# Kernel optimization log

Hardware: AMD Instinct MI355X
Metric: run time of the kernel (lower is better)

The kernel has to match this reference:

```python
import jax, jax.numpy as jnp
import numpy as np

NUM_HEAD = 8
EPS = 1e-12  # matches torch F.normalize default eps


def setup_inputs() -> dict:
    key = jax.random.key(0)
    k1, k2, k3 = jax.random.split(key, 3)
    B, N, C = 8, 8192, 384
    x = jax.random.normal(k1, (B, N, C), dtype=jnp.float32)
    # torch Linear weights: (out_features, in_features)
    w_qkv = jax.random.normal(k2, (3 * C, C), dtype=jnp.float32) * (C ** -0.5)
    w_proj = jax.random.normal(k3, (C, C), dtype=jnp.float32) * (C ** -0.5)
    b_proj = jnp.zeros((C,), dtype=jnp.float32)
    return {"x": x, "w_qkv": w_qkv, "w_proj": w_proj, "b_proj": b_proj}


def _l2norm(t):
    # F.normalize(t, dim=-1): t / max(||t||_2, eps)
    n = jnp.sqrt(jnp.sum(t * t, axis=-1, keepdims=True))
    return t / jnp.maximum(n, EPS)


def reference(x, w_qkv, w_proj, b_proj):
    B, N, C = x.shape
    H = NUM_HEAD
    Dh = C // H
    qkv = x @ w_qkv.T  # (B, N, 3C), qkv_bias=False
    qkv = qkv.reshape(B, N, 3, H, Dh).transpose(2, 0, 3, 1, 4)  # (3, B, H, N, Dh)
    q, k, v = qkv[0], qkv[1], qkv[2]
    # transpose(-2, -1) -> (B, H, Dh, N); normalize along N (cross-covariance attn)
    q = _l2norm(jnp.swapaxes(q, -2, -1))
    k = _l2norm(jnp.swapaxes(k, -2, -1))
    v = jnp.swapaxes(v, -2, -1)  # (B, H, Dh, N)
    attn = jnp.einsum('bhdn,bhen->bhde', q, k)  # (B, H, Dh, Dh)
    attn = jax.nn.softmax(attn, axis=-1)
    out = jnp.einsum('bhde,bhen->bhdn', attn, v)  # (B, H, Dh, N)
    out = out.transpose(0, 3, 1, 2).reshape(B, N, C)  # (B, N, C)
    out = out @ w_proj.T + b_proj
    return out
```

## Files before the change

### kernel.cpp

```cpp
#include <hip/hip_runtime.h>
#include <hip/hip_bf16.h>
#include <stdint.h>


typedef __bf16 bf16_t;
typedef __attribute__((ext_vector_type(8))) __bf16 bf16x8;
typedef __attribute__((ext_vector_type(4))) __bf16 bf16x4;
typedef __attribute__((ext_vector_type(4))) float f32x4;

#define NTOK 8192
#define CDIM 384
#define WH   25165824
#define DHN  393216

#define XCHUNKS 3145728
#define TCHUNKS 3201024

__device__ __forceinline__ f32x4 mfma16(bf16x8 a, bf16x8 b, f32x4 c) {
  return __builtin_amdgcn_mfma_f32_16x16x32_bf16(a, b, c, 0, 0, 0);
}

__device__ __forceinline__ void gload16(bf16_t* lds, const bf16_t* g) {
  __builtin_amdgcn_global_load_lds(
      (const __attribute__((address_space(1))) void*)g,
      (__attribute__((address_space(3))) void*)lds, 16, 0, 0);
}

template <bool BF16>
__device__ __forceinline__ bf16x8 load8(const void* p, int idx) {
  if constexpr (BF16) {
    return *(const bf16x8*)((const bf16_t*)p + idx);
  } else {
    const float* f = (const float*)p + idx;
    f32x4 a = *(const f32x4*)f;
    f32x4 b = *(const f32x4*)(f + 4);
    bf16x8 r;
    r[0] = (bf16_t)a[0]; r[1] = (bf16_t)a[1]; r[2] = (bf16_t)a[2]; r[3] = (bf16_t)a[3];
    r[4] = (bf16_t)b[0]; r[5] = (bf16_t)b[1]; r[6] = (bf16_t)b[2]; r[7] = (bf16_t)b[3];
    return r;
  }
}

__global__ void k_probe(const uint32_t* __restrict__ X, int* __restrict__ flag) {
  __shared__ int cnt;
  if (threadIdx.x == 0) cnt = 0;
  __syncthreads();
  const uint32_t w = X[threadIdx.x];
  const int e = (int)((w >> 7) & 0xFF);
  const int sane = (e >= 110 && e <= 131) ? 1 : 0;
  atomicAdd(&cnt, sane);
  __syncthreads();
  if (threadIdx.x == 0) *flag = (cnt >= 128) ? 1 : 0;
}

__global__ void k_zero(float* __restrict__ p, int n) {
  int i = blockIdx.x * 256 + threadIdx.x;
  if (i < n) p[i] = 0.f;
}

__global__ void k_cvt(const void* __restrict__ X, const void* __restrict__ Wqkv,
                      bf16_t* __restrict__ Xb, bf16_t* __restrict__ Wb,
                      const int* __restrict__ flagp) {
  const int isb = *flagp;
  const int G = gridDim.x * 256;
  for (int c = blockIdx.x * 256 + threadIdx.x; c < TCHUNKS; c += G) {
    const bool isX = c < XCHUNKS;
    const int lc = isX ? c : c - XCHUNKS;
    const void* src = isX ? X : Wqkv;
    bf16_t* dst = (isX ? Xb : Wb) + (size_t)lc * 8;
    if (isb) {
      *(bf16x8*)dst = *((const bf16x8*)src + lc);
    } else {
      const f32x4 a = *((const f32x4*)src + lc * 2);
      const f32x4 b = *((const f32x4*)src + lc * 2 + 1);
      bf16x8 r;
      r[0] = (bf16_t)a[0]; r[1] = (bf16_t)a[1]; r[2] = (bf16_t)a[2]; r[3] = (bf16_t)a[3];
      r[4] = (bf16_t)b[0]; r[5] = (bf16_t)b[1]; r[6] = (bf16_t)b[2]; r[7] = (bf16_t)b[3];
      *(bf16x8*)dst = r;
    }
  }
}

__device__ __forceinline__ void qkv_body_pipe(const bf16_t* __restrict__ XB,
                                              const bf16_t* __restrict__ WB,
                                              bf16_t* __restrict__ qkv,
                                              bf16_t* As, bf16_t* Bs) {
  const int tid = threadIdx.x;
  const int lane = tid & 63;
  const int wr = tid >> 7, wc = (tid >> 6) & 1;
  const int q4 = lane >> 4, l16 = lane & 15;
  const int rowB0 = blockIdx.x * 128;
  const int r0 = tid >> 2, kk = (tid & 3) << 3;
  const int bb = rowB0 >> 13;
  const int nB = rowB0 & 8191;

  auto STAGE = [&](int jts, int ks, int nxt) {
    const int rowA0 = jts * 128;
    const int k0 = ks * 32;
    bf16_t* Ad = As + nxt * 4096;
    bf16_t* Bd = Bs + nxt * 4096;
    gload16(Ad + tid * 8,         WB + (rowA0 + r0) * CDIM + k0 + kk);
    gload16(Ad + (tid + 256) * 8, WB + (rowA0 + r0 + 64) * CDIM + k0 + kk);
    gload16(Bd + tid * 8,         XB + (rowB0 + r0) * CDIM + k0 + kk);
    gload16(Bd + (tid + 256) * 8, XB + (rowB0 + r0 + 64) * CDIM + k0 + kk);
  };

  STAGE(0, 0, 0);
  __syncthreads();
  int cur = 0;

  for (int jt = 0; jt < 9; jt++) {
    const int which = jt / 3;
    const int jtt = jt - which * 3;
    f32x4 acc[4][4];
#pragma unroll
    for (int i = 0; i < 4; i++)
#pragma unroll
      for (int j = 0; j < 4; j++) acc[i][j] = (f32x4){0.f, 0.f, 0.f, 0.f};

    for (int k = 0; k < 12; k++) {
      if (!(jt == 8 && k == 11)) {
        int kn = k + 1, jn = jt;
        if (kn == 12) { kn = 0; jn = jt + 1; }
        STAGE(jn, kn, cur ^ 1);
      }
      const bf16_t* Ac = As + cur * 4096;
      const bf16_t* Bc = Bs + cur * 4096;
      bf16x8 af[4], bfr[4];
#pragma unroll
      for (int i = 0; i < 4; i++) {
        af[i]  = *(const bf16x8*)&Ac[(wr * 64 + i * 16 + l16) * 32 + q4 * 8];
        bfr[i] = *(const bf16x8*)&Bc[(wc * 64 + i * 16 + l16) * 32 + q4 * 8];
      }
      if (which < 2) {
#pragma unroll
        for (int i = 0; i < 4; i++)
#pragma unroll
          for (int j = 0; j < 4; j++) acc[i][j] = mfma16(bfr[j], af[i], acc[i][j]);
      } else {
#pragma unroll
        for (int i = 0; i < 4; i++)
#pragma unroll
          for (int j = 0; j < 4; j++) acc[i][j] = mfma16(af[i], bfr[j], acc[i][j]);
      }
      __syncthreads();
      cur ^= 1;
    }

    if (which < 2) {
#pragma unroll
      for (int i = 0; i < 4; i++) {
        const int rin = jtt * 128 + wr * 64 + i * 16 + l16;
        const int h = rin / 48, dh = rin - h * 48;
        bf16_t* rowp = qkv + which * WH + (bb * 8 + h) * DHN + dh * NTOK
                       + nB + wc * 64 + q4 * 4;
#pragma unroll
        for (int j = 0; j < 4; j++) {
          bf16x4 o = {(bf16_t)acc[i][j][0], (bf16_t)acc[i][j][1],
                      (bf16_t)acc[i][j][2], (bf16_t)acc[i][j][3]};
          *(bf16x4*)(rowp + j * 16) = o;
        }
      }
    } else {
#pragma unroll
      for (int i = 0; i < 4; i++) {
        const int rin0 = jtt * 128 + wr * 64 + i * 16 + q4 * 4;
#pragma unroll
        for (int j = 0; j < 4; j++) {
          const int mg = rowB0 + wc * 64 + j * 16 + l16;
          bf16x4 o = {(bf16_t)acc[i][j][0], (bf16_t)acc[i][j][1],
                      (bf16_t)acc[i][j][2], (bf16_t)acc[i][j][3]};
          *(bf16x4*)(qkv + 2 * WH + mg * CDIM + rin0) = o;
        }
      }
    }
  }
}

__global__ __launch_bounds__(256, 2) void k_gemm_qkv(
    const bf16_t* __restrict__ Xb, const bf16_t* __restrict__ Wb,
    bf16_t* __restrict__ qkv) {
  __shared__ __align__(16) bf16_t As[2 * 4096];
  __shared__ __align__(16) bf16_t Bs[2 * 4096];
  qkv_body_pipe(Xb, Wb, qkv, As, Bs);
}

template <bool BF16>
__device__ __forceinline__ void qkv_body_legacy(const void* __restrict__ X,
                                                const void* __restrict__ Wqkv,
                                                bf16_t* __restrict__ qkv,
                                                bf16_t* As, bf16_t* Bs) {
  const int tid = threadIdx.x;
  const int lane = tid & 63;
  const int wr = tid >> 7, wc = (tid >> 6) & 1;
  const int q4 = lane >> 4, l16 = lane & 15;
  const int rowB0 = blockIdx.x * 128;
  const int r0 = tid >> 2, kk = (tid & 3) << 3;
  const int bb = rowB0 >> 13;
  const int nB = rowB0 & 8191;

  for (int jt = 0; jt < 9; jt++) {
    const int rowA0 = jt * 128;
    const int which = jt / 3;
    const int jtt = jt - which * 3;
    f32x4 acc[4][4];
#pragma unroll
    for (int i = 0; i < 4; i++)
#pragma unroll
      for (int j = 0; j < 4; j++) acc[i][j] = (f32x4){0.f, 0.f, 0.f, 0.f};

    for (int k0 = 0; k0 < CDIM; k0 += 32) {
      bf16x8 a0 = load8<BF16>(Wqkv, (rowA0 + r0) * CDIM + k0 + kk);
      bf16x8 a1 = load8<BF16>(Wqkv, (rowA0 + r0 + 64) * CDIM + k0 + kk);
      bf16x8 b0 = load8<BF16>(X, (rowB0 + r0) * CDIM + k0 + kk);
      bf16x8 b1 = load8<BF16>(X, (rowB0 + r0 + 64) * CDIM + k0 + kk);
      __syncthreads();
      *(bf16x8*)&As[tid * 8] = a0;
      *(bf16x8*)&As[(tid + 256) * 8] = a1;
      *(bf16x8*)&Bs[tid * 8] = b0;
      *(bf16x8*)&Bs[(tid + 256) * 8] = b1;
      __syncthreads();
      bf16x8 af[4], bfr[4];
#pragma unroll
      for (int i = 0; i < 4; i++) {
        af[i]  = *(const bf16x8*)&As[(wr * 64 + i * 16 + l16) * 32 + q4 * 8];
        bfr[i] = *(const bf16x8*)&Bs[(wc * 64 + i * 16 + l16) * 32 + q4 * 8];
      }
      if (which < 2) {
#pragma unroll
        for (int i = 0; i < 4; i++)
#pragma unroll
          for (int j = 0; j < 4; j++) acc[i][j] = mfma16(bfr[j], af[i], acc[i][j]);
      } else {
#pragma unroll
        for (int i = 0; i < 4; i++)
#pragma unroll
          for (int j = 0; j < 4; j++) acc[i][j] = mfma16(af[i], bfr[j], acc[i][j]);
      }
    }

    if (which < 2) {
#pragma unroll
      for (int i = 0; i < 4; i++) {
        const int rin = jtt * 128 + wr * 64 + i * 16 + l16;
        const int h = rin / 48, dh = rin - h * 48;
        bf16_t* rowp = qkv + which * WH + (bb * 8 + h) * DHN + dh * NTOK
                       + nB + wc * 64 + q4 * 4;
#pragma unroll
        for (int j = 0; j < 4; j++) {
          bf16x4 o = {(bf16_t)acc[i][j][0], (bf16_t)acc[i][j][1],
                      (bf16_t)acc[i][j][2], (bf16_t)acc[i][j][3]};
          *(bf16x4*)(rowp + j * 16) = o;
        }
      }
    } else {
#pragma unroll
      for (int i = 0; i < 4; i++) {
        const int rin0 = jtt * 128 + wr * 64 + i * 16 + q4 * 4;
#pragma unroll
        for (int j = 0; j < 4; j++) {
          const int mg = rowB0 + wc * 64 + j * 16 + l16;
          bf16x4 o = {(bf16_t)acc[i][j][0], (bf16_t)acc[i][j][1],
                      (bf16_t)acc[i][j][2], (bf16_t)acc[i][j][3]};
          *(bf16x4*)(qkv + 2 * WH + mg * CDIM + rin0) = o;
        }
      }
    }
  }
}

__global__ __launch_bounds__(256, 2) void k_gemm_qkv_bf16(
    const void* __restrict__ X, const void* __restrict__ Wqkv,
    bf16_t* __restrict__ qkv, const int* __restrict__ flagp) {
  __shared__ __align__(16) bf16_t As[128 * 32];
  __shared__ __align__(16) bf16_t Bs[128 * 32];
  if (!*flagp) return;
  qkv_body_legacy<true>(X, Wqkv, qkv, As, Bs);
}

__global__ __launch_bounds__(256, 2) void k_gemm_qkv_f32(
    const void* __restrict__ X, const void* __restrict__ Wqkv,
    bf16_t* __restrict__ qkv, const int* __restrict__ flagp) {
  __shared__ __align__(16) bf16_t As[128 * 32];
  __shared__ __align__(16) bf16_t Bs[128 * 32];
  if (*flagp) return;
  qkv_body_legacy<false>(X, Wqkv, qkv, As, Bs);
}

__global__ __launch_bounds__(256, 2) void k_gram(
    const bf16_t* __restrict__ qkv, float* __restrict__ S_acc, float* __restrict__ ssq_acc) {
  __shared__ __align__(16) float sm[9312];
  bf16_t* Qs = (bf16_t*)sm;
  bf16_t* Ks = Qs + 6144;
  float* ssq_sm = sm + 9216;

  const int tid = threadIdx.x;
  const int wave = tid >> 6, lane = tid & 63, q4 = lane >> 4, l16 = lane & 15;
  const int s = blockIdx.x, bh = blockIdx.y;
  const bf16_t* Qg = qkv + bh * DHN;
  const bf16_t* Kg = qkv + WH + bh * DHN;

  if (tid < 96) ssq_sm[tid] = 0.f;

  f32x4 acc[3][3];
#pragma unroll
  for (int i = 0; i < 3; i++)
#pragma unroll
    for (int j = 0; j < 3; j++) acc[i][j] = (f32x4){0.f, 0.f, 0.f, 0.f};
  float qss[3] = {0.f, 0.f, 0.f}, kss[3] = {0.f, 0.f, 0.f};

  for (int t0 = 0; t0 < 8; t0++) {
    const int n0 = s * 1024 + t0 * 128;
    bf16x8 qv[3], kv[3];
#pragma unroll
    for (int jj = 0; jj < 3; jj++) {
      const int c = jj * 256 + tid;
      const int st = c / 192, rem = c - st * 192;
      const int row = rem >> 2, kk = (rem & 3) << 3;
      const int gofs = row * NTOK + n0 + st * 32 + kk;
      qv[jj] = *(const bf16x8*)(Qg + gofs);
      kv[jj] = *(const bf16x8*)(Kg + gofs);
    }
    __syncthreads();
#pragma unroll
    for (int jj = 0; jj < 3; jj++) {
      *(bf16x8*)&Qs[(jj * 256 + tid) * 8] = qv[jj];
      *(bf16x8*)&Ks[(jj * 256 + tid) * 8] = kv[jj];
    }
    __syncthreads();
    bf16x8 qf[3], kf[3];
#pragma unroll
    for (int i = 0; i < 3; i++) {
      qf[i] = *(const bf16x8*)&Qs[wave * 1536 + (i * 16 + l16) * 32 + q4 * 8];
      kf[i] = *(const bf16x8*)&Ks[wave * 1536 + (i * 16 + l16) * 32 + q4 * 8];
    }
#pragma unroll
    for (int i = 0; i < 3; i++) {
#pragma unroll
      for (int u = 0; u < 8; u++) {
        const float qv2 = (float)qf[i][u], kv2 = (float)kf[i][u];
        qss[i] += qv2 * qv2;
        kss[i] += kv2 * kv2;
      }
#pragma unroll
      for (int j = 0; j < 3; j++) acc[i][j] = mfma16(qf[i], kf[j], acc[i][j]);
    }
  }

  __syncthreads();
  float* red = sm;
#pragma unroll
  for (int i = 0; i < 3; i++)
#pragma unroll
    for (int j = 0; j < 3; j++)
#pragma unroll
      for (int r = 0; r < 4; r++)
        red[wave * 2304 + (i * 3 + j) * 256 + lane * 4 + r] = acc[i][j][r];
#pragma unroll
  for (int i = 0; i < 3; i++) {
    atomicAdd(&ssq_sm[i * 16 + l16], qss[i]);
    atomicAdd(&ssq_sm[48 + i * 16 + l16], kss[i]);
  }
  __syncthreads();
  for (int idx = tid; idx < 2304; idx += 256) {
    const float v = red[idx] + red[2304 + idx] + red[4608 + idx] + red[6912 + idx];
    const int tile = idx >> 8, ln = (idx >> 2) & 63, r = idx & 3;
    const int i = tile / 3, j = tile - i * 3;
    const int d = i * 16 + ((ln >> 4) << 2) + r;
    const int e = j * 16 + (ln & 15);
    atomicAdd(&S_acc[bh * 2304 + d * 48 + e], v);
  }
  if (tid < 96) atomicAdd(&ssq_acc[bh * 96 + tid], ssq_sm[tid]);
}

__global__ void k_softmax(const float* __restrict__ S_acc, const float* __restrict__ ssq_acc,
                          float* __restrict__ attn_f) {
  __shared__ float invk_sm[48];
  const int bh = blockIdx.x, d = threadIdx.x;
  if (d < 48) invk_sm[d] = 1.f / fmaxf(sqrtf(ssq_acc[bh * 96 + 48 + d]), 1e-12f);
  __syncthreads();
  if (d < 48) {
    const float invq = 1.f / fmaxf(sqrtf(ssq_acc[bh * 96 + d]), 1e-12f);
    float lg[48], mx = -1e30f;
#pragma unroll
    for (int e = 0; e < 48; e++) {
      lg[e] = S_acc[bh * 2304 + d * 48 + e] * invq * invk_sm[e];
      mx = fmaxf(mx, lg[e]);
    }
    float ssum = 0.f;
#pragma unroll
    for (int e = 0; e < 48; e++) { lg[e] = expf(lg[e] - mx); ssum += lg[e]; }
    const float inv = 1.f / ssum;
#pragma unroll
    for (int e = 0; e < 48; e++) attn_f[bh * 2304 + d * 48 + e] = lg[e] * inv;
  }
}

__global__ void k_weff(
    const float* __restrict__ attn_f, const void* __restrict__ Wp,
    bf16_t* __restrict__ Weff, const int* __restrict__ flagp) {
  __shared__ float a_sm[2304];
  __shared__ float w_sm[2304];
  const int isb = *flagp;
  const int bid = blockIdx.x;
  const int ct = bid & 7, h = (bid >> 3) & 7, b = bid >> 6;
  const int bh = b * 8 + h;
  const int tid = threadIdx.x;

  for (int i = tid; i < 2304; i += 256) {
    a_sm[i] = attn_f[bh * 2304 + i];
    const int r = i / 48, c = i - r * 48;
    const int gi = (ct * 48 + r) * CDIM + h * 48 + c;
    w_sm[i] = isb ? (float)((const bf16_t*)Wp)[gi] : ((const float*)Wp)[gi];
  }
  __syncthreads();

  for (int o = tid; o < 2304; o += 256) {
    const int r = o / 48, e = o - r * 48;
    float s = 0.f;
#pragma unroll 8
    for (int d = 0; d < 48; d++) s += w_sm[r * 48 + d] * a_sm[d * 48 + e];
    Weff[b * 147456 + (ct * 48 + r) * CDIM + h * 48 + e] = (bf16_t)s;
  }
}

__global__ __launch_bounds__(256, 2) void k_gemm_out(
    const bf16_t* __restrict__ Weff, const bf16_t* __restrict__ qkv,
    const void* __restrict__ bias, void* __restrict__ out, const int* __restrict__ flagp) {
  __shared__ __align__(16) bf16_t As[2 * 4096];
  __shared__ __align__(16) bf16_t Bs[2 * 4096];
  const int isb = *flagp;
  const int tid = threadIdx.x;
  const int lane = tid & 63;
  const int wr = tid >> 7, wc = (tid >> 6) & 1;
  const int q4 = lane >> 4, l16 = lane & 15;
  const int b = blockIdx.y;
  const int rowB0 = blockIdx.x * 128;
  const bf16_t* Aa = Weff + b * 147456;
  const bf16_t* Ba = qkv + 2 * WH + b * (NTOK * CDIM);
  const int r0 = tid >> 2, kk = (tid & 3) << 3;

  auto STAGE = [&](int cts, int ks, int nxt) {
    const int rowA0 = cts * 128;
    const int k0 = ks * 32;
    bf16_t* Ad = As + nxt * 4096;
    bf16_t* Bd = Bs + nxt * 4096;
    gload16(Ad + tid * 8,         Aa + (rowA0 + r0) * CDIM + k0 + kk);
    gload16(Ad + (tid + 256) * 8, Aa + (rowA0 + r0 + 64) * CDIM + k0 + kk);
    gload16(Bd + tid * 8,         Ba + (rowB0 + r0) * CDIM + k0 + kk);
    gload16(Bd + (tid + 256) * 8, Ba + (rowB0 + r0 + 64) * CDIM + k0 + kk);
  };

  STAGE(0, 0, 0);
  __syncthreads();
  int cur = 0;

  for (int ct = 0; ct < 3; ct++) {
    const int rowA0 = ct * 128;
    f32x4 acc[4][4];
#pragma unroll
    for (int i = 0; i < 4; i++)
#pragma unroll
      for (int j = 0; j < 4; j++) acc[i][j] = (f32x4){0.f, 0.f, 0.f, 0.f};

    for (int k = 0; k < 12; k++) {
      if (!(ct == 2 && k == 11)) {
        int kn = k + 1, cn = ct;
        if (kn == 12) { kn = 0; cn = ct + 1; }
        STAGE(cn, kn, cur ^ 1);
      }
      const bf16_t* Ac = As + cur * 4096;
      const bf16_t* Bc = Bs + cur * 4096;
      bf16x8 af[4], bfr[4];
#pragma unroll
      for (int i = 0; i < 4; i++) {
        af[i]  = *(const bf16x8*)&Ac[(wr * 64 + i * 16 + l16) * 32 + q4 * 8];
        bfr[i] = *(const bf16x8*)&Bc[(wc * 64 + i * 16 + l16) * 32 + q4 * 8];
      }
#pragma unroll
      for (int i = 0; i < 4; i++)
#pragma unroll
        for (int j = 0; j < 4; j++) acc[i][j] = mfma16(af[i], bfr[j], acc[i][j]);
      __syncthreads();
      cur ^= 1;
    }

#pragma unroll
    for (int i = 0; i < 4; i++) {
      const int cg = rowA0 + wr * 64 + i * 16 + q4 * 4;
      float bv[4];
#pragma unroll
      for (int r = 0; r < 4; r++)
        bv[r] = isb ? (float)((const bf16_t*)bias)[cg + r] : ((const float*)bias)[cg + r];
#pragma unroll
      for (int j = 0; j < 4; j++) {
        const int ng = rowB0 + wc * 64 + j * 16 + l16;
        const int oi = (b * NTOK + ng) * CDIM + cg;
        if (isb) {
          bf16x4 o = {(bf16_t)(acc[i][j][0] + bv[0]), (bf16_t)(acc[i][j][1] + bv[1]),
                      (bf16_t)(acc[i][j][2] + bv[2]), (bf16_t)(acc[i][j][3] + bv[3])};
          *(bf16x4*)((bf16_t*)out + oi) = o;
        } else {
          f32x4 o = {acc[i][j][0] + bv[0], acc[i][j][1] + bv[1],
                     acc[i][j][2] + bv[2], acc[i][j][3] + bv[3]};
          *(f32x4*)((float*)out + oi) = o;
        }
      }
    }
  }
}

extern "C" void kernel_launch(void* const* d_in, const int* in_sizes, int n_in,
                              void* d_out, int out_size, void* d_ws, size_t ws_size,
                              hipStream_t stream) {
  (void)in_sizes; (void)n_in; (void)out_size;
  const void* X    = d_in[0];
  const void* Wqkv = d_in[1];
  const void* Wp   = d_in[2];
  const void* bias = d_in[3];

  char* ws = (char*)d_ws;
  bf16_t* qkv    = (bf16_t*)ws;
  float*  S_acc  = (float*)(ws + 150994944);
  float*  ssq    = (float*)(ws + 151584768);
  float*  attn_f = (float*)(ws + 151609344);
  bf16_t* Weff   = (bf16_t*)(ws + 152199168);
  int*    flag   = (int*)(ws + 154558464);
  bf16_t* Xb     = (bf16_t*)(ws + 154558720);
  bf16_t* Wb     = (bf16_t*)(ws + 204890368);

  const bool have_cvt_ws = ws_size >= 205775104ULL;

  k_probe<<<dim3(1), 256, 0, stream>>>((const uint32_t*)X, flag);
  k_zero<<<dim3(600), 256, 0, stream>>>(S_acc, 153600);
  if (have_cvt_ws) {
    k_cvt<<<dim3(2048), 256, 0, stream>>>(X, Wqkv, Xb, Wb, flag);
    k_gemm_qkv<<<dim3(512), 256, 0, stream>>>(Xb, Wb, qkv);
  } else {
    k_gemm_qkv_bf16<<<dim3(512), 256, 0, stream>>>(X, Wqkv, qkv, flag);
    k_gemm_qkv_f32<<<dim3(512), 256, 0, stream>>>(X, Wqkv, qkv, flag);
  }
  k_gram<<<dim3(8, 64), 256, 0, stream>>>(qkv, S_acc, ssq);
  k_softmax<<<dim3(64), 64, 0, stream>>>(S_acc, ssq, attn_f);
  k_weff<<<dim3(512), 256, 0, stream>>>(attn_f, Wp, Weff, flag);
  k_gemm_out<<<dim3(64, 8), 256, 0, stream>>>(Weff, qkv, bias, d_out, flag);
}
```

Baseline: 408.8 us.

## Pre-swizzle operands into MFMA fragment layout and stream weights from global

The conversion kernel now writes X and W_qkv in a tiled fragment order (16 rows by 32 k, lane-major) so each lane's bf16x8 MFMA operand is one contiguous 16-byte load. The QKV GEMM now loads the block's full 64-token X strip into LDS once and reads weight fragments straight from global memory, which removes the double-buffered staging and the per-k-step barriers. Tiles shrink to 64 tokens with 1024 blocks and a launch bound of 3 blocks per CU. In exchange, weights are re-read from global/L2 by every block, and each wave does less MFMA work per load.

```diff
diff --git a/kernel.cpp b/kernel.cpp
--- a/kernel.cpp
+++ b/kernel.cpp
@@ -59,20 +59,26 @@
 }
 
 __global__ void k_cvt(const void* __restrict__ X, const void* __restrict__ Wqkv,
-                      bf16_t* __restrict__ Xb, bf16_t* __restrict__ Wb,
+                      bf16_t* __restrict__ Xf, bf16_t* __restrict__ Wf,
                       const int* __restrict__ flagp) {
   const int isb = *flagp;
   const int G = gridDim.x * 256;
   for (int c = blockIdx.x * 256 + threadIdx.x; c < TCHUNKS; c += G) {
     const bool isX = c < XCHUNKS;
     const int lc = isX ? c : c - XCHUNKS;
+    const int t = lc >> 6, ln = lc & 63;
+    const int tm = t / 12, tk = t - tm * 12;
+    const int m = tm * 16 + (ln & 15);
+    const int k = tk * 32 + ((ln >> 4) << 3);
+    const int off = m * CDIM + k;
     const void* src = isX ? X : Wqkv;
-    bf16_t* dst = (isX ? Xb : Wb) + (size_t)lc * 8;
+    bf16_t* dst = (isX ? Xf : Wf) + (size_t)lc * 8;
     if (isb) {
-      *(bf16x8*)dst = *((const bf16x8*)src + lc);
+      *(bf16x8*)dst = *(const bf16x8*)((const bf16_t*)src + off);
     } else {
-      const f32x4 a = *((const f32x4*)src + lc * 2);
-      const f32x4 b = *((const f32x4*)src + lc * 2 + 1);
+      const float* f = (const float*)src + off;
+      const f32x4 a = *(const f32x4*)f;
+      const f32x4 b = *(const f32x4*)(f + 4);
       bf16x8 r;
       r[0] = (bf16_t)a[0]; r[1] = (bf16_t)a[1]; r[2] = (bf16_t)a[2]; r[3] = (bf16_t)a[3];
       r[4] = (bf16_t)b[0]; r[5] = (bf16_t)b[1]; r[6] = (bf16_t)b[2]; r[7] = (bf16_t)b[3];
@@ -81,79 +87,66 @@
   }
 }
 
-__device__ __forceinline__ void qkv_body_pipe(const bf16_t* __restrict__ XB,
-                                              const bf16_t* __restrict__ WB,
-                                              bf16_t* __restrict__ qkv,
-                                              bf16_t* As, bf16_t* Bs) {
+__global__ __launch_bounds__(256, 3) void k_gemm_qkv(
+    const bf16_t* __restrict__ Xf, const bf16_t* __restrict__ Wf,
+    bf16_t* __restrict__ qkv) {
+  __shared__ __align__(16) bf16_t Bs[24576];
+
   const int tid = threadIdx.x;
   const int lane = tid & 63;
-  const int wr = tid >> 7, wc = (tid >> 6) & 1;
+  const int wv = tid >> 6;
   const int q4 = lane >> 4, l16 = lane & 15;
-  const int rowB0 = blockIdx.x * 128;
-  const int r0 = tid >> 2, kk = (tid & 3) << 3;
-  const int bb = rowB0 >> 13;
-  const int nB = rowB0 & 8191;
-
-  auto STAGE = [&](int jts, int ks, int nxt) {
-    const int rowA0 = jts * 128;
-    const int k0 = ks * 32;
-    bf16_t* Ad = As + nxt * 4096;
-    bf16_t* Bd = Bs + nxt * 4096;
-    gload16(Ad + tid * 8,         WB + (rowA0 + r0) * CDIM + k0 + kk);
-    gload16(Ad + (tid + 256) * 8, WB + (rowA0 + r0 + 64) * CDIM + k0 + kk);
-    gload16(Bd + tid * 8,         XB + (rowB0 + r0) * CDIM + k0 + kk);
-    gload16(Bd + (tid + 256) * 8, XB + (rowB0 + r0 + 64) * CDIM + k0 + kk);
-  };
-
-  STAGE(0, 0, 0);
-  __syncthreads();
-  int cur = 0;
+  const int tok0 = blockIdx.x * 64;
+  const int bb = tok0 >> 13;
+  const int nB = tok0 & 8191;
+
+  const bf16_t* Bsrc = Xf + (size_t)tok0 * CDIM;
+#pragma unroll
+  for (int s = 0; s < 12; s++) {
+    const int chunk = s * 256 + tid;
+    gload16(Bs + chunk * 8, Bsrc + chunk * 8);
+  }
+  __syncthreads();
 
   for (int jt = 0; jt < 9; jt++) {
     const int which = jt / 3;
     const int jtt = jt - which * 3;
-    f32x4 acc[4][4];
-#pragma unroll
-    for (int i = 0; i < 4; i++)
+    f32x4 acc[2][4];
+#pragma unroll
+    for (int i = 0; i < 2; i++)
 #pragma unroll
       for (int j = 0; j < 4; j++) acc[i][j] = (f32x4){0.f, 0.f, 0.f, 0.f};
 
-    for (int k = 0; k < 12; k++) {
-      if (!(jt == 8 && k == 11)) {
-        int kn = k + 1, jn = jt;
-        if (kn == 12) { kn = 0; jn = jt + 1; }
-        STAGE(jn, kn, cur ^ 1);
-      }
-      const bf16_t* Ac = As + cur * 4096;
-      const bf16_t* Bc = Bs + cur * 4096;
-      bf16x8 af[4], bfr[4];
-#pragma unroll
-      for (int i = 0; i < 4; i++) {
-        af[i]  = *(const bf16x8*)&Ac[(wr * 64 + i * 16 + l16) * 32 + q4 * 8];
-        bfr[i] = *(const bf16x8*)&Bc[(wc * 64 + i * 16 + l16) * 32 + q4 * 8];
-      }
+    const int rt0 = jt * 8 + wv * 2;
+#pragma unroll 2
+    for (int kc = 0; kc < 12; kc++) {
+      bf16x8 af[2], bfr[4];
+#pragma unroll
+      for (int i = 0; i < 2; i++)
+        af[i] = *(const bf16x8*)(Wf + (size_t)((rt0 + i) * 12 + kc) * 512 + lane * 8);
+#pragma unroll
+      for (int j = 0; j < 4; j++)
+        bfr[j] = *(const bf16x8*)&Bs[(j * 12 + kc) * 512 + lane * 8];
       if (which < 2) {
 #pragma unroll
-        for (int i = 0; i < 4; i++)
+        for (int i = 0; i < 2; i++)
 #pragma unroll
           for (int j = 0; j < 4; j++) acc[i][j] = mfma16(bfr[j], af[i], acc[i][j]);
       } else {
 #pragma unroll
-        for (int i = 0; i < 4; i++)
+        for (int i = 0; i < 2; i++)
 #pragma unroll
           for (int j = 0; j < 4; j++) acc[i][j] = mfma16(af[i], bfr[j], acc[i][j]);
       }
-      __syncthreads();
-      cur ^= 1;
     }
 
     if (which < 2) {
 #pragma unroll
-      for (int i = 0; i < 4; i++) {
-        const int rin = jtt * 128 + wr * 64 + i * 16 + l16;
+      for (int i = 0; i < 2; i++) {
+        const int rin = jtt * 128 + wv * 32 + i * 16 + l16;
         const int h = rin / 48, dh = rin - h * 48;
         bf16_t* rowp = qkv + which * WH + (bb * 8 + h) * DHN + dh * NTOK
-                       + nB + wc * 64 + q4 * 4;
+                       + nB + q4 * 4;
 #pragma unroll
         for (int j = 0; j < 4; j++) {
           bf16x4 o = {(bf16_t)acc[i][j][0], (bf16_t)acc[i][j][1],
@@ -163,26 +156,18 @@
       }
     } else {
 #pragma unroll
-      for (int i = 0; i < 4; i++) {
-        const int rin0 = jtt * 128 + wr * 64 + i * 16 + q4 * 4;
+      for (int i = 0; i < 2; i++) {
+        const int c0 = jtt * 128 + wv * 32 + i * 16 + q4 * 4;
 #pragma unroll
         for (int j = 0; j < 4; j++) {
-          const int mg = rowB0 + wc * 64 + j * 16 + l16;
+          const int mg = tok0 + j * 16 + l16;
           bf16x4 o = {(bf16_t)acc[i][j][0], (bf16_t)acc[i][j][1],
                       (bf16_t)acc[i][j][2], (bf16_t)acc[i][j][3]};
-          *(bf16x4*)(qkv + 2 * WH + mg * CDIM + rin0) = o;
+          *(bf16x4*)(qkv + 2 * WH + (size_t)mg * CDIM + c0) = o;
         }
       }
     }
   }
-}
-
-__global__ __launch_bounds__(256, 2) void k_gemm_qkv(
-    const bf16_t* __restrict__ Xb, const bf16_t* __restrict__ Wb,
-    bf16_t* __restrict__ qkv) {
-  __shared__ __align__(16) bf16_t As[2 * 4096];
-  __shared__ __align__(16) bf16_t Bs[2 * 4096];
-  qkv_body_pipe(Xb, Wb, qkv, As, Bs);
 }
 
 template <bool BF16>
@@ -526,16 +511,16 @@
   float*  attn_f = (float*)(ws + 151609344);
   bf16_t* Weff   = (bf16_t*)(ws + 152199168);
   int*    flag   = (int*)(ws + 154558464);
-  bf16_t* Xb     = (bf16_t*)(ws + 154558720);
-  bf16_t* Wb     = (bf16_t*)(ws + 204890368);
+  bf16_t* Xf     = (bf16_t*)(ws + 154558720);
+  bf16_t* Wf     = (bf16_t*)(ws + 204890368);
 
   const bool have_cvt_ws = ws_size >= 205775104ULL;
 
   k_probe<<<dim3(1), 256, 0, stream>>>((const uint32_t*)X, flag);
   k_zero<<<dim3(600), 256, 0, stream>>>(S_acc, 153600);
   if (have_cvt_ws) {
-    k_cvt<<<dim3(2048), 256, 0, stream>>>(X, Wqkv, Xb, Wb, flag);
-    k_gemm_qkv<<<dim3(512), 256, 0, stream>>>(Xb, Wb, qkv);
+    k_cvt<<<dim3(2048), 256, 0, stream>>>(X, Wqkv, Xf, Wf, flag);
+    k_gemm_qkv<<<dim3(1024), 256, 0, stream>>>(Xf, Wf, qkv);
   } else {
     k_gemm_qkv_bf16<<<dim3(512), 256, 0, stream>>>(X, Wqkv, qkv, flag);
     k_gemm_qkv_f32<<<dim3(512), 256, 0, stream>>>(X, Wqkv, qkv, flag);
```

New measurement: 394.0 us. 1.04x faster.
